# Performance work log

Hardware: AMD Instinct MI355X
Metric: run time of the kernel (lower is better)

Reference implementation:

```python
import jax, jax.numpy as jnp
import numpy as np

V_NUM = 50000
E_NUM = 10000
EMB_DIM = 128
LAYER_NUM = 2
N_INC = 600000
VE_TAU = 1.0
EV_TAU = 1.0


def _segment_softmax(a, idx, num_segments):
    # a: [N, 1], idx: [N] -> softmax within each segment (stable)
    m = jax.ops.segment_max(a, idx, num_segments=num_segments)
    ex = jnp.exp(a - m[idx])
    s = jax.ops.segment_sum(ex, idx, num_segments=num_segments)
    return ex / s[idx]


def setup_inputs() -> dict:
    key = jax.random.key(0)
    ks = jax.random.split(key, 12)
    std = (2.0 ** 0.5) * (2.0 / (EMB_DIM + 1)) ** 0.5  # xavier_normal gain sqrt(2)
    v_emb = jax.random.normal(ks[0], (V_NUM, EMB_DIM), dtype=jnp.float32)
    t_emb = jax.random.normal(ks[1], (V_NUM, EMB_DIM), dtype=jnp.float32)
    e_emb = jax.random.normal(ks[2], (E_NUM, EMB_DIM), dtype=jnp.float32)
    v_idx = jax.random.randint(ks[3], (N_INC, 1), 0, V_NUM)
    e_idx = jax.random.randint(ks[4], (N_INC, 1), 0, E_NUM)
    ve = jnp.concatenate([v_idx, e_idx], axis=1).astype(jnp.int32)
    p = lambda k: std * jax.random.normal(k, (LAYER_NUM, EMB_DIM), dtype=jnp.float32)
    return {
        "v_emb": v_emb, "t_emb": t_emb, "e_emb": e_emb, "ve": ve,
        "av_v2e": p(ks[5]), "at_v2e": p(ks[6]), "ae_v2e": p(ks[7]),
        "av_e2v": p(ks[8]), "at_e2v": p(ks[9]), "ae_e2v": p(ks[10]),
    }


def _agg(v_fea, t_fea, e_fea, v, e, av, at, ae, tau, dst_idx, dst_num, src_fea, src_idx):
    # attention logits per incidence: tanh(a_v[v] + a_t[v] + a_e[e]) / tau, shape [N, 1]
    sv = v_fea @ av[:, None]  # [V,1]
    st = t_fea @ at[:, None]  # [V,1]
    se = e_fea @ ae[:, None]  # [E,1]
    a = jnp.tanh(sv[v] + st[v] + se[e]) / tau
    a = _segment_softmax(a, dst_idx, dst_num)
    return jax.ops.segment_sum(a * src_fea[src_idx], dst_idx, num_segments=dst_num)


def reference(v_emb, t_emb, e_emb, ve, av_v2e, at_v2e, ae_v2e, av_e2v, at_e2v, ae_e2v):
    v = ve[:, 0]
    e = ve[:, 1]
    v_stack = [v_emb]
    e_stack = [e_emb]
    for l in range(LAYER_NUM):
        v_fea = v_stack[-1]
        e_fea = e_stack[-1]
        # V2E: softmax over edge segments, aggregate node features into edges
        e_new = _agg(v_fea, t_emb, e_fea, v, e, av_v2e[l], at_v2e[l], ae_v2e[l],
                     VE_TAU, e, E_NUM, v_fea, v)
        e_stack.append(jax.nn.relu(e_new))
        # E2V uses pre-relu e_new (as in original: e_fea_ not reassigned to relu)
        v_new = _agg(v_fea, t_emb, e_new, v, e, av_e2v[l], at_e2v[l], ae_e2v[l],
                     EV_TAU, v, V_NUM, e_new, e)
        v_stack.append(jax.nn.relu(v_new))
    v_out = jnp.mean(jnp.stack(v_stack, axis=1), axis=1)
    e_out = jnp.mean(jnp.stack(e_stack, axis=1), axis=1)
    return (v_out, e_out)
```

## Files before the change

### kernel.cpp

```cpp
#include <hip/hip_runtime.h>

#define DIM 128
#define VSTRIDE 48
#define ESTRIDE 128
#define NSL 128
#define DSLE 79
#define DSLV 391
#define CAPS 5440

typedef unsigned short ushort_t;
typedef unsigned int   uint_t;

__device__ inline ushort_t f2bf(float f) {
    uint_t u = __float_as_uint(f);
    u += 0x7FFF + ((u >> 16) & 1);
    return (ushort_t)(u >> 16);
}
__device__ inline float bf2f(ushort_t h) { return __uint_as_float((uint_t)h << 16); }
__device__ inline float lo16(uint_t u) { return bf2f((ushort_t)u); }
__device__ inline float hi16(uint_t u) { return bf2f((ushort_t)(u >> 16)); }

__device__ inline float wfun(float x) {
    float t = __expf(2.f * x);
    float r = __builtin_amdgcn_rcpf(t + 1.f);
    return __expf(1.f - 2.f * r);
}

__device__ inline float wred(float x) {
    #pragma unroll
    for (int o = 32; o; o >>= 1) x += __shfl_xor(x, o, 64);
    return x;
}

__global__ void k_part(const int2* __restrict__ ve, int N,
                       int* __restrict__ curE, int* __restrict__ curV,
                       uint_t* __restrict__ peE, uint_t* __restrict__ peV)
{
    __shared__ int hE[NSL], hV[NSL], baE[NSL], baV[NSL];
    int k0 = blockIdx.x * 1024;
    int k1 = min(N, k0 + 1024);
    if (threadIdx.x < NSL) { hE[threadIdx.x] = 0; }
    else if (threadIdx.x < 2 * NSL) { hV[threadIdx.x - NSL] = 0; }
    __syncthreads();
    for (int k = k0 + threadIdx.x; k < k1; k += 256) {
        int2 p = ve[k];
        atomicAdd(&hE[(uint_t)p.y / DSLE], 1);
        atomicAdd(&hV[(uint_t)p.x / DSLV], 1);
    }
    __syncthreads();
    if (threadIdx.x < NSL) {
        int t = threadIdx.x;
        baE[t] = atomicAdd(&curE[t], hE[t]); hE[t] = 0;
    } else if (threadIdx.x < 2 * NSL) {
        int t = threadIdx.x - NSL;
        baV[t] = atomicAdd(&curV[t], hV[t]); hV[t] = 0;
    }
    __syncthreads();
    for (int k = k0 + threadIdx.x; k < k1; k += 256) {
        int2 p = ve[k];
        uint_t sE = (uint_t)p.y / DSLE, sV = (uint_t)p.x / DSLV;
        int rE = baE[sE] + atomicAdd(&hE[sE], 1);
        if (rE < CAPS)
            peE[(size_t)sE * CAPS + rE] = ((uint_t)(p.y - sE * DSLE) << 16) | (uint_t)p.x;
        int rV = baV[sV] + atomicAdd(&hV[sV], 1);
        if (rV < CAPS)
            peV[(size_t)sV * CAPS + rV] = ((uint_t)(p.x - sV * DSLV) << 16) | (uint_t)p.y;
    }
}

__global__ void k_setup(const uint_t* __restrict__ peE, const uint_t* __restrict__ peV,
                        const int* __restrict__ curE, const int* __restrict__ curV,
                        int* __restrict__ cntE, int* __restrict__ cntV,
                        ushort_t* __restrict__ bE, ushort_t* __restrict__ bV,
                        const float* __restrict__ v_emb, const float* __restrict__ t_emb,
                        const float* __restrict__ e_emb,
                        const float* __restrict__ av0, const float* __restrict__ at0,
                        const float* __restrict__ av1, const float* __restrict__ at1,
                        const float* __restrict__ at2, const float* __restrict__ at3,
                        const float* __restrict__ ae0,
                        uint_t* __restrict__ vb,
                        float* __restrict__ scv0, float* __restrict__ scv1,
                        float* __restrict__ st2, float* __restrict__ st3,
                        float* __restrict__ sce0,
                        int V, int E, int gVpre)
{
    __shared__ __align__(16) ushort_t sb[DSLV * VSTRIDE];
    __shared__ int shc[DSLV];
    int b = blockIdx.x;
    if (b < 2 * NSL) {
        int isV = (b >= NSL);
        int s = isV ? b - NSL : b;
        int dsl = isV ? DSLV : DSLE;
        int stride = isV ? VSTRIDE : ESTRIDE;
        int lo = s * dsl;
        int nd = min((isV ? V : E) - lo, dsl);
        if (nd <= 0) return;
        const uint_t* pe = (isV ? peV : peE) + (size_t)s * CAPS;
        int len = (isV ? curV : curE)[s]; if (len > CAPS) len = CAPS;
        for (int t = threadIdx.x; t < nd; t += 256) shc[t] = 0;
        __syncthreads();
        for (int i = threadIdx.x; i < len; i += 256) {
            uint_t u = pe[i];
            int dl = (int)(u >> 16);
            int slot = atomicAdd(&shc[dl], 1);
            if (slot < stride) sb[dl * stride + slot] = (ushort_t)(u & 0xffffu);
        }
        __syncthreads();
        int* cnt = isV ? cntV : cntE;
        for (int t = threadIdx.x; t < nd; t += 256) cnt[lo + t] = shc[t];
        uint_t* gout = (uint_t*)((isV ? bV : bE) + (size_t)lo * stride);
        const uint_t* lsrc = (const uint_t*)sb;
        int nu = nd * stride / 2;
        for (int t = threadIdx.x; t < nu; t += 256) gout[t] = lsrc[t];
        return;
    }
    b -= 2 * NSL;
    int lane = threadIdx.x & 63;
    int wv   = threadIdx.x >> 6;
    if (b < gVpre) {
        int row = b * 4 + wv;
        if (row >= V) return;
        float2 v = ((const float2*)(v_emb + (size_t)row * DIM))[lane];
        float2 t = ((const float2*)(t_emb + (size_t)row * DIM))[lane];
        vb[(size_t)row * 64 + lane] = (uint_t)f2bf(v.x) | ((uint_t)f2bf(v.y) << 16);
        float2 a0 = ((const float2*)av0)[lane], b0 = ((const float2*)at0)[lane];
        float2 a1 = ((const float2*)av1)[lane], b1 = ((const float2*)at1)[lane];
        float2 b2 = ((const float2*)at2)[lane], b3 = ((const float2*)at3)[lane];
        float d0 = v.x * a0.x + v.y * a0.y + t.x * b0.x + t.y * b0.y;
        float d1 = v.x * a1.x + v.y * a1.y + t.x * b1.x + t.y * b1.y;
        float d2 = t.x * b2.x + t.y * b2.y;
        float d3 = t.x * b3.x + t.y * b3.y;
        d0 = wred(d0); d1 = wred(d1); d2 = wred(d2); d3 = wred(d3);
        if (lane == 0) { scv0[row] = d0; scv1[row] = d1; st2[row] = d2; st3[row] = d3; }
    } else {
        int row = (b - gVpre) * 4 + wv;
        if (row >= E) return;
        float2 v = ((const float2*)(e_emb + (size_t)row * DIM))[lane];
        float2 a = ((const float2*)ae0)[lane];
        float d = wred(v.x * a.x + v.y * a.y);
        if (lane == 0) sce0[row] = d;
    }
}

__global__ void k_gatherE(const ushort_t* __restrict__ bucket, const int* __restrict__ cnt,
                          const float* __restrict__ scSrc, const float* __restrict__ scDst,
                          const uint_t* __restrict__ src_bf,
                          float* __restrict__ outF, uint_t* __restrict__ outB, int reluB,
                          const float* __restrict__ pd0, float* __restrict__ osc0,
                          const float* __restrict__ pd1, float* __restrict__ osc1, int relu1,
                          const float* __restrict__ meanA, const float* __restrict__ meanB,
                          int ndst)
{
    __shared__ float l4[4][32][4];
    __shared__ float lw[4];
    int dst = blockIdx.x;
    if (dst >= ndst) return;
    int wv = threadIdx.x >> 6, lane = threadIdx.x & 63;
    int h = lane >> 5, c = lane & 31;
    int m = cnt[dst]; if (m > ESTRIDE) m = ESTRIDE;
    const ushort_t* s = bucket + (size_t)dst * ESTRIDE;
    float sd = scDst[dst];
    int m4 = (m + 3) >> 2;
    int j0 = wv * m4;
    int cw = min(m, j0 + m4) - j0; if (cw < 0) cw = 0;
    int   idxl = 0;
    float wl   = 0.f;
    if (lane < cw) {
        idxl = s[j0 + lane];
        wl   = wfun(scSrc[idxl] + sd);
    }
    float ws = wred(wl);
    float a0 = 0.f, a1 = 0.f, a2 = 0.f, a3 = 0.f;
    int mp = (cw + 3) & ~3;
    for (int j = 0; j < mp; j += 4) {
        int   i0 = __shfl(idxl, j + h, 64),     i1 = __shfl(idxl, j + 2 + h, 64);
        float w0 = __shfl(wl,   j + h, 64),     w1 = __shfl(wl,   j + 2 + h, 64);
        uint2 u0 = ((const uint2*)(src_bf + (size_t)i0 * 64))[c];
        uint2 u1 = ((const uint2*)(src_bf + (size_t)i1 * 64))[c];
        a0 += w0 * lo16(u0.x) + w1 * lo16(u1.x);
        a1 += w0 * hi16(u0.x) + w1 * hi16(u1.x);
        a2 += w0 * lo16(u0.y) + w1 * lo16(u1.y);
        a3 += w0 * hi16(u0.y) + w1 * hi16(u1.y);
    }
    a0 += __shfl_xor(a0, 32, 64); a1 += __shfl_xor(a1, 32, 64);
    a2 += __shfl_xor(a2, 32, 64); a3 += __shfl_xor(a3, 32, 64);
    if (lane < 32) { l4[wv][c][0] = a0; l4[wv][c][1] = a1; l4[wv][c][2] = a2; l4[wv][c][3] = a3; }
    if (lane == 0) lw[wv] = ws;
    __syncthreads();
    if (wv != 0) return;
    bool act = lane < 32;
    a0 = l4[0][c][0] + l4[1][c][0] + l4[2][c][0] + l4[3][c][0];
    a1 = l4[0][c][1] + l4[1][c][1] + l4[2][c][1] + l4[3][c][1];
    a2 = l4[0][c][2] + l4[1][c][2] + l4[2][c][2] + l4[3][c][2];
    a3 = l4[0][c][3] + l4[1][c][3] + l4[2][c][3] + l4[3][c][3];
    ws = lw[0] + lw[1] + lw[2] + lw[3];
    float inv = (ws > 0.f) ? 1.f / ws : 0.f;
    float4 r; r.x = a0 * inv; r.y = a1 * inv; r.z = a2 * inv; r.w = a3 * inv;
    if (outB && act) {
        float bx = reluB ? fmaxf(r.x, 0.f) : r.x, by = reluB ? fmaxf(r.y, 0.f) : r.y;
        float bz = reluB ? fmaxf(r.z, 0.f) : r.z, bw = reluB ? fmaxf(r.w, 0.f) : r.w;
        uint2 u; u.x = (uint_t)f2bf(bx) | ((uint_t)f2bf(by) << 16);
        u.y = (uint_t)f2bf(bz) | ((uint_t)f2bf(bw) << 16);
        ((uint2*)(outB + (size_t)dst * 64))[c] = u;
    }
    if (pd0) {
        float4 q = ((const float4*)pd0)[c];
        float d = act ? (r.x * q.x + r.y * q.y + r.z * q.z + r.w * q.w) : 0.f;
        d = wred(d);
        if (lane == 0) osc0[dst] = d;
    }
    if (pd1) {
        float x0 = relu1 ? fmaxf(r.x, 0.f) : r.x, x1 = relu1 ? fmaxf(r.y, 0.f) : r.y;
        float x2 = relu1 ? fmaxf(r.z, 0.f) : r.z, x3 = relu1 ? fmaxf(r.w, 0.f) : r.w;
        float4 q = ((const float4*)pd1)[c];
        float d = act ? (x0 * q.x + x1 * q.y + x2 * q.z + x3 * q.w) : 0.f;
        d = wred(d);
        if (lane == 0) osc1[dst] = d;
    }
    if (meanA) {
        float4 ma = ((const float4*)(meanA + (size_t)dst * DIM))[c];
        float4 mb = ((const float4*)(meanB + (size_t)dst * DIM))[c];
        r.x = (ma.x + fmaxf(mb.x, 0.f) + fmaxf(r.x, 0.f)) * (1.f / 3.f);
        r.y = (ma.y + fmaxf(mb.y, 0.f) + fmaxf(r.y, 0.f)) * (1.f / 3.f);
        r.z = (ma.z + fmaxf(mb.z, 0.f) + fmaxf(r.z, 0.f)) * (1.f / 3.f);
        r.w = (ma.w + fmaxf(mb.w, 0.f) + fmaxf(r.w, 0.f)) * (1.f / 3.f);
    }
    if (act) ((float4*)(outF + (size_t)dst * DIM))[c] = r;
}

__global__ void k_gatherV(const ushort_t* __restrict__ bucket, const int* __restrict__ cnt,
                          const float* __restrict__ scSrc, const float* __restrict__ scDst,
                          const uint_t* __restrict__ src_bf,
                          float* __restrict__ outF, uint_t* __restrict__ outB, int reluB,
                          const float* __restrict__ pd0, const float* __restrict__ sta0,
                          float* __restrict__ osc0, int relu0,
                          const float* __restrict__ pd1, const float* __restrict__ sta1,
                          float* __restrict__ osc1, int relu1,
                          const float* __restrict__ meanA, const float* __restrict__ meanB,
                          int ndst)
{
    int dst  = blockIdx.x * 4 + (threadIdx.x >> 6);
    int lane = threadIdx.x & 63;
    int h = lane >> 5, c = lane & 31;
    if (dst >= ndst) return;
    int m = cnt[dst]; if (m > VSTRIDE) m = VSTRIDE;
    const ushort_t* s = bucket + (size_t)dst * VSTRIDE;
    float sd = scDst[dst];
    int   idxl = 0;
    float wl   = 0.f;
    if (lane < m) {
        idxl = s[lane];
        wl   = wfun(scSrc[idxl] + sd);
    }
    float ws = wred(wl);
    float a0 = 0.f, a1 = 0.f, a2 = 0.f, a3 = 0.f;
    int mp = (m + 3) & ~3;
    for (int j = 0; j < mp; j += 4) {
        int   i0 = __shfl(idxl, j + h, 64),     i1 = __shfl(idxl, j + 2 + h, 64);
        float w0 = __shfl(wl,   j + h, 64),     w1 = __shfl(wl,   j + 2 + h, 64);
        uint2 u0 = ((const uint2*)(src_bf + (size_t)i0 * 64))[c];
        uint2 u1 = ((const uint2*)(src_bf + (size_t)i1 * 64))[c];
        a0 += w0 * lo16(u0.x) + w1 * lo16(u1.x);
        a1 += w0 * hi16(u0.x) + w1 * hi16(u1.x);
        a2 += w0 * lo16(u0.y) + w1 * lo16(u1.y);
        a3 += w0 * hi16(u0.y) + w1 * hi16(u1.y);
    }
    a0 += __shfl_xor(a0, 32, 64); a1 += __shfl_xor(a1, 32, 64);
    a2 += __shfl_xor(a2, 32, 64); a3 += __shfl_xor(a3, 32, 64);
    bool act = lane < 32;
    float inv = (ws > 0.f) ? 1.f / ws : 0.f;
    float4 r; r.x = a0 * inv; r.y = a1 * inv; r.z = a2 * inv; r.w = a3 * inv;
    if (outB && act) {
        float bx = reluB ? fmaxf(r.x, 0.f) : r.x, by = reluB ? fmaxf(r.y, 0.f) : r.y;
        float bz = reluB ? fmaxf(r.z, 0.f) : r.z, bw = reluB ? fmaxf(r.w, 0.f) : r.w;
        uint2 u; u.x = (uint_t)f2bf(bx) | ((uint_t)f2bf(by) << 16);
        u.y = (uint_t)f2bf(bz) | ((uint_t)f2bf(bw) << 16);
        ((uint2*)(outB + (size_t)dst * 64))[c] = u;
    }
    if (pd0) {
        float x0 = relu0 ? fmaxf(r.x, 0.f) : r.x, x1 = relu0 ? fmaxf(r.y, 0.f) : r.y;
        float x2 = relu0 ? fmaxf(r.z, 0.f) : r.z, x3 = relu0 ? fmaxf(r.w, 0.f) : r.w;
        float4 q = ((const float4*)pd0)[c];
        float d = act ? (x0 * q.x + x1 * q.y + x2 * q.z + x3 * q.w) : 0.f;
        d = wred(d);
        if (lane == 0) osc0[dst] = d + (sta0 ? sta0[dst] : 0.f);
    }
    if (pd1) {
        float x0 = relu1 ? fmaxf(r.x, 0.f) : r.x, x1 = relu1 ? fmaxf(r.y, 0.f) : r.y;
        float x2 = relu1 ? fmaxf(r.z, 0.f) : r.z, x3 = relu1 ? fmaxf(r.w, 0.f) : r.w;
        float4 q = ((const float4*)pd1)[c];
        float d = act ? (x0 * q.x + x1 * q.y + x2 * q.z + x3 * q.w) : 0.f;
        d = wred(d);
        if (lane == 0) osc1[dst] = d + (sta1 ? sta1[dst] : 0.f);
    }
    if (meanA) {
        float4 ma = ((const float4*)(meanA + (size_t)dst * DIM))[c];
        float4 mb = ((const float4*)(meanB + (size_t)dst * DIM))[c];
        r.x = (ma.x + fmaxf(mb.x, 0.f) + fmaxf(r.x, 0.f)) * (1.f / 3.f);
        r.y = (ma.y + fmaxf(mb.y, 0.f) + fmaxf(r.y, 0.f)) * (1.f / 3.f);
        r.z = (ma.z + fmaxf(mb.z, 0.f) + fmaxf(r.z, 0.f)) * (1.f / 3.f);
        r.w = (ma.w + fmaxf(mb.w, 0.f) + fmaxf(r.w, 0.f)) * (1.f / 3.f);
    }
    if (act) ((float4*)(outF + (size_t)dst * DIM))[c] = r;
}

extern "C" void kernel_launch(void* const* d_in, const int* in_sizes, int n_in,
                              void* d_out, int out_size, void* d_ws, size_t ws_size,
                              hipStream_t stream)
{
    const float* v_emb  = (const float*)d_in[0];
    const float* t_emb  = (const float*)d_in[1];
    const float* e_emb  = (const float*)d_in[2];
    const int2*  ve     = (const int2*)d_in[3];
    const float* av_v2e = (const float*)d_in[4];
    const float* at_v2e = (const float*)d_in[5];
    const float* ae_v2e = (const float*)d_in[6];
    const float* av_e2v = (const float*)d_in[7];
    const float* at_e2v = (const float*)d_in[8];
    const float* ae_e2v = (const float*)d_in[9];

    const int V = in_sizes[0] / DIM;
    const int E = in_sizes[2] / DIM;
    const int N = in_sizes[3] / 2;

    char* p = (char*)d_ws;
    auto alloc = [&](size_t bytes) { char* r = p; p += (bytes + 255) & ~(size_t)255; return r; };
    float* v_new0 = (float*)alloc((size_t)V * DIM * 4);
    float* e_new0 = (float*)alloc((size_t)E * DIM * 4);
    uint_t* vb    = (uint_t*)alloc((size_t)V * 64 * 4);
    uint_t* eb    = (uint_t*)alloc((size_t)E * 64 * 4);
    ushort_t* bV  = (ushort_t*)alloc((size_t)V * VSTRIDE * 2);
    ushort_t* bE  = (ushort_t*)alloc((size_t)E * ESTRIDE * 2);
    uint_t* peE   = (uint_t*)alloc((size_t)NSL * CAPS * 4);
    uint_t* peV   = (uint_t*)alloc((size_t)NSL * CAPS * 4);
    int*   cntV   = (int*)alloc((size_t)(V + E + 2 * NSL) * 4);
    int*   cntE   = cntV + V;
    int*   curE   = cntE + E;
    int*   curV   = curE + NSL;
    float* scv0   = (float*)alloc((size_t)V * 4);
    float* scv1   = (float*)alloc((size_t)V * 4);
    float* scv2   = (float*)alloc((size_t)V * 4);
    float* scv3   = (float*)alloc((size_t)V * 4);
    float* st2    = (float*)alloc((size_t)V * 4);
    float* st3    = (float*)alloc((size_t)V * 4);
    float* sce0   = (float*)alloc((size_t)E * 4);
    float* sce1   = (float*)alloc((size_t)E * 4);
    float* sce2   = (float*)alloc((size_t)E * 4);
    float* sce3   = (float*)alloc((size_t)E * 4);

    float* out_v = (float*)d_out;
    float* out_e = out_v + (size_t)V * DIM;

    hipMemsetAsync(curE, 0, (size_t)2 * NSL * 4, stream);

    k_part<<<(N + 1023) / 1024, 256, 0, stream>>>(ve, N, curE, curV, peE, peV);

    const int gVpre = (V + 3) / 4, gEpre = (E + 3) / 4;
    k_setup<<<2 * NSL + gVpre + gEpre, 256, 0, stream>>>(
        peE, peV, curE, curV, cntE, cntV, bE, bV,
        v_emb, t_emb, e_emb,
        av_v2e, at_v2e, av_e2v, at_e2v, at_v2e + DIM, at_e2v + DIM, ae_v2e,
        vb, scv0, scv1, st2, st3, sce0, V, E, gVpre);

    k_gatherE<<<E, 256, 0, stream>>>(bE, cntE, scv0, sce0, vb,
        e_new0, eb, 0, ae_e2v, sce1, ae_v2e + DIM, sce2, 1,
        nullptr, nullptr, E);

    k_gatherV<<<(V + 3) / 4, 256, 0, stream>>>(bV, cntV, sce1, scv1, eb,
        v_new0, vb, 1,
        av_v2e + DIM, st2, scv2, 1,
        av_e2v + DIM, st3, scv3, 1,
        nullptr, nullptr, V);

    k_gatherE<<<E, 256, 0, stream>>>(bE, cntE, scv2, sce2, vb,
        out_e, eb, 0, ae_e2v + DIM, sce3, nullptr, nullptr, 0,
        e_emb, e_new0, E);

    k_gatherV<<<(V + 3) / 4, 256, 0, stream>>>(bV, cntV, sce3, scv3, eb,
        out_v, nullptr, 0,
        nullptr, nullptr, nullptr, 0,
        nullptr, nullptr, nullptr, 0,
        v_emb, v_new0, V);
}
```

Before: 171.7 us.

## Remap gather kernels: one wave per edge, two vertices per wave

The edge gather now gives each edge a single wavefront instead of a 256-thread block. Each lane holds up to two incidences, which removes the shared-memory cross-wave reduction and the block barrier. The vertex gather now processes two vertices per wavefront with interleaved loads, raising memory-level parallelism and amortising per-wave setup. The shared epilogue moves into a helper function. Risks: the edge path is now serialized over about 60 incidences per wave, and two accumulator sets raise register pressure.

```diff
diff --git a/kernel.cpp b/kernel.cpp
--- a/kernel.cpp
+++ b/kernel.cpp
@@ -142,6 +142,49 @@
     }
 }
 
+__device__ inline void epilog(int dst, int lane, int c, float4 r,
+                              float* __restrict__ outF, uint_t* __restrict__ outB, int reluB,
+                              const float* __restrict__ pd0, const float* __restrict__ sta0,
+                              float* __restrict__ osc0, int relu0,
+                              const float* __restrict__ pd1, const float* __restrict__ sta1,
+                              float* __restrict__ osc1, int relu1,
+                              const float* __restrict__ meanA, const float* __restrict__ meanB)
+{
+    bool act = lane < 32;
+    if (outB && act) {
+        float bx = reluB ? fmaxf(r.x, 0.f) : r.x, by = reluB ? fmaxf(r.y, 0.f) : r.y;
+        float bz = reluB ? fmaxf(r.z, 0.f) : r.z, bw = reluB ? fmaxf(r.w, 0.f) : r.w;
+        uint2 u; u.x = (uint_t)f2bf(bx) | ((uint_t)f2bf(by) << 16);
+        u.y = (uint_t)f2bf(bz) | ((uint_t)f2bf(bw) << 16);
+        ((uint2*)(outB + (size_t)dst * 64))[c] = u;
+    }
+    if (pd0) {
+        float x0 = relu0 ? fmaxf(r.x, 0.f) : r.x, x1 = relu0 ? fmaxf(r.y, 0.f) : r.y;
+        float x2 = relu0 ? fmaxf(r.z, 0.f) : r.z, x3 = relu0 ? fmaxf(r.w, 0.f) : r.w;
+        float4 q = ((const float4*)pd0)[c];
+        float d = act ? (x0 * q.x + x1 * q.y + x2 * q.z + x3 * q.w) : 0.f;
+        d = wred(d);
+        if (lane == 0) osc0[dst] = d + (sta0 ? sta0[dst] : 0.f);
+    }
+    if (pd1) {
+        float x0 = relu1 ? fmaxf(r.x, 0.f) : r.x, x1 = relu1 ? fmaxf(r.y, 0.f) : r.y;
+        float x2 = relu1 ? fmaxf(r.z, 0.f) : r.z, x3 = relu1 ? fmaxf(r.w, 0.f) : r.w;
+        float4 q = ((const float4*)pd1)[c];
+        float d = act ? (x0 * q.x + x1 * q.y + x2 * q.z + x3 * q.w) : 0.f;
+        d = wred(d);
+        if (lane == 0) osc1[dst] = d + (sta1 ? sta1[dst] : 0.f);
+    }
+    if (meanA) {
+        float4 ma = ((const float4*)(meanA + (size_t)dst * DIM))[c];
+        float4 mb = ((const float4*)(meanB + (size_t)dst * DIM))[c];
+        r.x = (ma.x + fmaxf(mb.x, 0.f) + fmaxf(r.x, 0.f)) * (1.f / 3.f);
+        r.y = (ma.y + fmaxf(mb.y, 0.f) + fmaxf(r.y, 0.f)) * (1.f / 3.f);
+        r.z = (ma.z + fmaxf(mb.z, 0.f) + fmaxf(r.z, 0.f)) * (1.f / 3.f);
+        r.w = (ma.w + fmaxf(mb.w, 0.f) + fmaxf(r.w, 0.f)) * (1.f / 3.f);
+    }
+    if (act) ((float4*)(outF + (size_t)dst * DIM))[c] = r;
+}
+
 __global__ void k_gatherE(const ushort_t* __restrict__ bucket, const int* __restrict__ cnt,
                           const float* __restrict__ scSrc, const float* __restrict__ scDst,
                           const uint_t* __restrict__ src_bf,
@@ -151,81 +194,43 @@
                           const float* __restrict__ meanA, const float* __restrict__ meanB,
                           int ndst)
 {
-    __shared__ float l4[4][32][4];
-    __shared__ float lw[4];
-    int dst = blockIdx.x;
+    int dst  = blockIdx.x * 4 + (threadIdx.x >> 6);
+    int lane = threadIdx.x & 63;
+    int h = lane >> 5, c = lane & 31;
     if (dst >= ndst) return;
-    int wv = threadIdx.x >> 6, lane = threadIdx.x & 63;
-    int h = lane >> 5, c = lane & 31;
     int m = cnt[dst]; if (m > ESTRIDE) m = ESTRIDE;
     const ushort_t* s = bucket + (size_t)dst * ESTRIDE;
     float sd = scDst[dst];
-    int m4 = (m + 3) >> 2;
-    int j0 = wv * m4;
-    int cw = min(m, j0 + m4) - j0; if (cw < 0) cw = 0;
-    int   idxl = 0;
-    float wl   = 0.f;
-    if (lane < cw) {
-        idxl = s[j0 + lane];
-        wl   = wfun(scSrc[idxl] + sd);
-    }
-    float ws = wred(wl);
+    int idx0 = 0, idx1 = 0;
+    float w0l = 0.f, w1l = 0.f;
+    if (lane < m)      { idx0 = s[lane];      w0l = wfun(scSrc[idx0] + sd); }
+    if (64 + lane < m) { idx1 = s[64 + lane]; w1l = wfun(scSrc[idx1] + sd); }
+    float ws = wred(w0l + w1l);
     float a0 = 0.f, a1 = 0.f, a2 = 0.f, a3 = 0.f;
-    int mp = (cw + 3) & ~3;
+    int mp = (m + 3) & ~3;
     for (int j = 0; j < mp; j += 4) {
-        int   i0 = __shfl(idxl, j + h, 64),     i1 = __shfl(idxl, j + 2 + h, 64);
-        float w0 = __shfl(wl,   j + h, 64),     w1 = __shfl(wl,   j + 2 + h, 64);
-        uint2 u0 = ((const uint2*)(src_bf + (size_t)i0 * 64))[c];
-        uint2 u1 = ((const uint2*)(src_bf + (size_t)i1 * 64))[c];
-        a0 += w0 * lo16(u0.x) + w1 * lo16(u1.x);
-        a1 += w0 * hi16(u0.x) + w1 * hi16(u1.x);
-        a2 += w0 * lo16(u0.y) + w1 * lo16(u1.y);
-        a3 += w0 * hi16(u0.y) + w1 * hi16(u1.y);
+        int jj = j & 63;
+        int ia, ib; float wa, wb;
+        if (j < 64) {
+            ia = __shfl(idx0, jj + h, 64);     wa = __shfl(w0l, jj + h, 64);
+            ib = __shfl(idx0, jj + 2 + h, 64); wb = __shfl(w0l, jj + 2 + h, 64);
+        } else {
+            ia = __shfl(idx1, jj + h, 64);     wa = __shfl(w1l, jj + h, 64);
+            ib = __shfl(idx1, jj + 2 + h, 64); wb = __shfl(w1l, jj + 2 + h, 64);
+        }
+        uint2 u0 = ((const uint2*)(src_bf + (size_t)ia * 64))[c];
+        uint2 u1 = ((const uint2*)(src_bf + (size_t)ib * 64))[c];
+        a0 += wa * lo16(u0.x) + wb * lo16(u1.x);
+        a1 += wa * hi16(u0.x) + wb * hi16(u1.x);
+        a2 += wa * lo16(u0.y) + wb * lo16(u1.y);
+        a3 += wa * hi16(u0.y) + wb * hi16(u1.y);
     }
     a0 += __shfl_xor(a0, 32, 64); a1 += __shfl_xor(a1, 32, 64);
     a2 += __shfl_xor(a2, 32, 64); a3 += __shfl_xor(a3, 32, 64);
-    if (lane < 32) { l4[wv][c][0] = a0; l4[wv][c][1] = a1; l4[wv][c][2] = a2; l4[wv][c][3] = a3; }
-    if (lane == 0) lw[wv] = ws;
-    __syncthreads();
-    if (wv != 0) return;
-    bool act = lane < 32;
-    a0 = l4[0][c][0] + l4[1][c][0] + l4[2][c][0] + l4[3][c][0];
-    a1 = l4[0][c][1] + l4[1][c][1] + l4[2][c][1] + l4[3][c][1];
-    a2 = l4[0][c][2] + l4[1][c][2] + l4[2][c][2] + l4[3][c][2];
-    a3 = l4[0][c][3] + l4[1][c][3] + l4[2][c][3] + l4[3][c][3];
-    ws = lw[0] + lw[1] + lw[2] + lw[3];
     float inv = (ws > 0.f) ? 1.f / ws : 0.f;
     float4 r; r.x = a0 * inv; r.y = a1 * inv; r.z = a2 * inv; r.w = a3 * inv;
-    if (outB && act) {
-        float bx = reluB ? fmaxf(r.x, 0.f) : r.x, by = reluB ? fmaxf(r.y, 0.f) : r.y;
-        float bz = reluB ? fmaxf(r.z, 0.f) : r.z, bw = reluB ? fmaxf(r.w, 0.f) : r.w;
-        uint2 u; u.x = (uint_t)f2bf(bx) | ((uint_t)f2bf(by) << 16);
-        u.y = (uint_t)f2bf(bz) | ((uint_t)f2bf(bw) << 16);
-        ((uint2*)(outB + (size_t)dst * 64))[c] = u;
-    }
-    if (pd0) {
-        float4 q = ((const float4*)pd0)[c];
-        float d = act ? (r.x * q.x + r.y * q.y + r.z * q.z + r.w * q.w) : 0.f;
-        d = wred(d);
-        if (lane == 0) osc0[dst] = d;
-    }
-    if (pd1) {
-        float x0 = relu1 ? fmaxf(r.x, 0.f) : r.x, x1 = relu1 ? fmaxf(r.y, 0.f) : r.y;
-        float x2 = relu1 ? fmaxf(r.z, 0.f) : r.z, x3 = relu1 ? fmaxf(r.w, 0.f) : r.w;
-        float4 q = ((const float4*)pd1)[c];
-        float d = act ? (x0 * q.x + x1 * q.y + x2 * q.z + x3 * q.w) : 0.f;
-        d = wred(d);
-        if (lane == 0) osc1[dst] = d;
-    }
-    if (meanA) {
-        float4 ma = ((const float4*)(meanA + (size_t)dst * DIM))[c];
-        float4 mb = ((const float4*)(meanB + (size_t)dst * DIM))[c];
-        r.x = (ma.x + fmaxf(mb.x, 0.f) + fmaxf(r.x, 0.f)) * (1.f / 3.f);
-        r.y = (ma.y + fmaxf(mb.y, 0.f) + fmaxf(r.y, 0.f)) * (1.f / 3.f);
-        r.z = (ma.z + fmaxf(mb.z, 0.f) + fmaxf(r.z, 0.f)) * (1.f / 3.f);
-        r.w = (ma.w + fmaxf(mb.w, 0.f) + fmaxf(r.w, 0.f)) * (1.f / 3.f);
-    }
-    if (act) ((float4*)(outF + (size_t)dst * DIM))[c] = r;
+    epilog(dst, lane, c, r, outF, outB, reluB,
+           pd0, nullptr, osc0, 0, pd1, nullptr, osc1, relu1, meanA, meanB);
 }
 
 __global__ void k_gatherV(const ushort_t* __restrict__ bucket, const int* __restrict__ cnt,
@@ -239,69 +244,59 @@
                           const float* __restrict__ meanA, const float* __restrict__ meanB,
                           int ndst)
 {
-    int dst  = blockIdx.x * 4 + (threadIdx.x >> 6);
+    int wv   = threadIdx.x >> 6;
     int lane = threadIdx.x & 63;
     int h = lane >> 5, c = lane & 31;
-    if (dst >= ndst) return;
-    int m = cnt[dst]; if (m > VSTRIDE) m = VSTRIDE;
-    const ushort_t* s = bucket + (size_t)dst * VSTRIDE;
-    float sd = scDst[dst];
-    int   idxl = 0;
-    float wl   = 0.f;
-    if (lane < m) {
-        idxl = s[lane];
-        wl   = wfun(scSrc[idxl] + sd);
-    }
-    float ws = wred(wl);
-    float a0 = 0.f, a1 = 0.f, a2 = 0.f, a3 = 0.f;
-    int mp = (m + 3) & ~3;
+    int dA = blockIdx.x * 8 + wv * 2;
+    int dB = dA + 1;
+    if (dA >= ndst) return;
+    bool hasB = dB < ndst;
+    int mA = cnt[dA]; if (mA > VSTRIDE) mA = VSTRIDE;
+    int mB = hasB ? cnt[dB] : 0; if (mB > VSTRIDE) mB = VSTRIDE;
+    const ushort_t* sA = bucket + (size_t)dA * VSTRIDE;
+    const ushort_t* sB = bucket + (size_t)dB * VSTRIDE;
+    float sdA = scDst[dA];
+    float sdB = hasB ? scDst[dB] : 0.f;
+    int idxA = 0, idxB = 0;
+    float wA = 0.f, wB = 0.f;
+    if (lane < mA) { idxA = sA[lane]; wA = wfun(scSrc[idxA] + sdA); }
+    if (lane < mB) { idxB = sB[lane]; wB = wfun(scSrc[idxB] + sdB); }
+    float wsA = wred(wA), wsB = wred(wB);
+    float aA0 = 0.f, aA1 = 0.f, aA2 = 0.f, aA3 = 0.f;
+    float aB0 = 0.f, aB1 = 0.f, aB2 = 0.f, aB3 = 0.f;
+    int mp = max((mA + 3) & ~3, (mB + 3) & ~3);
     for (int j = 0; j < mp; j += 4) {
-        int   i0 = __shfl(idxl, j + h, 64),     i1 = __shfl(idxl, j + 2 + h, 64);
-        float w0 = __shfl(wl,   j + h, 64),     w1 = __shfl(wl,   j + 2 + h, 64);
-        uint2 u0 = ((const uint2*)(src_bf + (size_t)i0 * 64))[c];
-        uint2 u1 = ((const uint2*)(src_bf + (size_t)i1 * 64))[c];
-        a0 += w0 * lo16(u0.x) + w1 * lo16(u1.x);
-        a1 += w0 * hi16(u0.x) + w1 * hi16(u1.x);
-        a2 += w0 * lo16(u0.y) + w1 * lo16(u1.y);
-        a3 += w0 * hi16(u0.y) + w1 * hi16(u1.y);
-    }
-    a0 += __shfl_xor(a0, 32, 64); a1 += __shfl_xor(a1, 32, 64);
-    a2 += __shfl_xor(a2, 32, 64); a3 += __shfl_xor(a3, 32, 64);
-    bool act = lane < 32;
-    float inv = (ws > 0.f) ? 1.f / ws : 0.f;
-    float4 r; r.x = a0 * inv; r.y = a1 * inv; r.z = a2 * inv; r.w = a3 * inv;
-    if (outB && act) {
-        float bx = reluB ? fmaxf(r.x, 0.f) : r.x, by = reluB ? fmaxf(r.y, 0.f) : r.y;
-        float bz = reluB ? fmaxf(r.z, 0.f) : r.z, bw = reluB ? fmaxf(r.w, 0.f) : r.w;
-        uint2 u; u.x = (uint_t)f2bf(bx) | ((uint_t)f2bf(by) << 16);
-        u.y = (uint_t)f2bf(bz) | ((uint_t)f2bf(bw) << 16);
-        ((uint2*)(outB + (size_t)dst * 64))[c] = u;
-    }
-    if (pd0) {
-        float x0 = relu0 ? fmaxf(r.x, 0.f) : r.x, x1 = relu0 ? fmaxf(r.y, 0.f) : r.y;
-        float x2 = relu0 ? fmaxf(r.z, 0.f) : r.z, x3 = relu0 ? fmaxf(r.w, 0.f) : r.w;
-        float4 q = ((const float4*)pd0)[c];
-        float d = act ? (x0 * q.x + x1 * q.y + x2 * q.z + x3 * q.w) : 0.f;
-        d = wred(d);
-        if (lane == 0) osc0[dst] = d + (sta0 ? sta0[dst] : 0.f);
-    }
-    if (pd1) {
-        float x0 = relu1 ? fmaxf(r.x, 0.f) : r.x, x1 = relu1 ? fmaxf(r.y, 0.f) : r.y;
-        float x2 = relu1 ? fmaxf(r.z, 0.f) : r.z, x3 = relu1 ? fmaxf(r.w, 0.f) : r.w;
-        float4 q = ((const float4*)pd1)[c];
-        float d = act ? (x0 * q.x + x1 * q.y + x2 * q.z + x3 * q.w) : 0.f;
-        d = wred(d);
-        if (lane == 0) osc1[dst] = d + (sta1 ? sta1[dst] : 0.f);
-    }
-    if (meanA) {
-        float4 ma = ((const float4*)(meanA + (size_t)dst * DIM))[c];
-        float4 mb = ((const float4*)(meanB + (size_t)dst * DIM))[c];
-        r.x = (ma.x + fmaxf(mb.x, 0.f) + fmaxf(r.x, 0.f)) * (1.f / 3.f);
-        r.y = (ma.y + fmaxf(mb.y, 0.f) + fmaxf(r.y, 0.f)) * (1.f / 3.f);
-        r.z = (ma.z + fmaxf(mb.z, 0.f) + fmaxf(r.z, 0.f)) * (1.f / 3.f);
-        r.w = (ma.w + fmaxf(mb.w, 0.f) + fmaxf(r.w, 0.f)) * (1.f / 3.f);
-    }
-    if (act) ((float4*)(outF + (size_t)dst * DIM))[c] = r;
+        int   iA0 = __shfl(idxA, j + h, 64),     iA1 = __shfl(idxA, j + 2 + h, 64);
+        float vA0 = __shfl(wA,   j + h, 64),     vA1 = __shfl(wA,   j + 2 + h, 64);
+        int   iB0 = __shfl(idxB, j + h, 64),     iB1 = __shfl(idxB, j + 2 + h, 64);
+        float vB0 = __shfl(wB,   j + h, 64),     vB1 = __shfl(wB,   j + 2 + h, 64);
+        uint2 uA0 = ((const uint2*)(src_bf + (size_t)iA0 * 64))[c];
+        uint2 uA1 = ((const uint2*)(src_bf + (size_t)iA1 * 64))[c];
+        uint2 uB0 = ((const uint2*)(src_bf + (size_t)iB0 * 64))[c];
+        uint2 uB1 = ((const uint2*)(src_bf + (size_t)iB1 * 64))[c];
+        aA0 += vA0 * lo16(uA0.x) + vA1 * lo16(uA1.x);
+        aA1 += vA0 * hi16(uA0.x) + vA1 * hi16(uA1.x);
+        aA2 += vA0 * lo16(uA0.y) + vA1 * lo16(uA1.y);
+        aA3 += vA0 * hi16(uA0.y) + vA1 * hi16(uA1.y);
+        aB0 += vB0 * lo16(uB0.x) + vB1 * lo16(uB1.x);
+        aB1 += vB0 * hi16(uB0.x) + vB1 * hi16(uB1.x);
+        aB2 += vB0 * lo16(uB0.y) + vB1 * lo16(uB1.y);
+        aB3 += vB0 * hi16(uB0.y) + vB1 * hi16(uB1.y);
+    }
+    aA0 += __shfl_xor(aA0, 32, 64); aA1 += __shfl_xor(aA1, 32, 64);
+    aA2 += __shfl_xor(aA2, 32, 64); aA3 += __shfl_xor(aA3, 32, 64);
+    aB0 += __shfl_xor(aB0, 32, 64); aB1 += __shfl_xor(aB1, 32, 64);
+    aB2 += __shfl_xor(aB2, 32, 64); aB3 += __shfl_xor(aB3, 32, 64);
+    float invA = (wsA > 0.f) ? 1.f / wsA : 0.f;
+    float4 rA; rA.x = aA0 * invA; rA.y = aA1 * invA; rA.z = aA2 * invA; rA.w = aA3 * invA;
+    epilog(dA, lane, c, rA, outF, outB, reluB,
+           pd0, sta0, osc0, relu0, pd1, sta1, osc1, relu1, meanA, meanB);
+    if (hasB) {
+        float invB = (wsB > 0.f) ? 1.f / wsB : 0.f;
+        float4 rB; rB.x = aB0 * invB; rB.y = aB1 * invB; rB.z = aB2 * invB; rB.w = aB3 * invB;
+        epilog(dB, lane, c, rB, outF, outB, reluB,
+               pd0, sta0, osc0, relu0, pd1, sta1, osc1, relu1, meanA, meanB);
+    }
 }
 
 extern "C" void kernel_launch(void* const* d_in, const int* in_sizes, int n_in,
@@ -362,21 +357,21 @@
         av_v2e, at_v2e, av_e2v, at_e2v, at_v2e + DIM, at_e2v + DIM, ae_v2e,
         vb, scv0, scv1, st2, st3, sce0, V, E, gVpre);
 
-    k_gatherE<<<E, 256, 0, stream>>>(bE, cntE, scv0, sce0, vb,
+    k_gatherE<<<(E + 3) / 4, 256, 0, stream>>>(bE, cntE, scv0, sce0, vb,
         e_new0, eb, 0, ae_e2v, sce1, ae_v2e + DIM, sce2, 1,
         nullptr, nullptr, E);
 
-    k_gatherV<<<(V + 3) / 4, 256, 0, stream>>>(bV, cntV, sce1, scv1, eb,
+    k_gatherV<<<(V + 7) / 8, 256, 0, stream>>>(bV, cntV, sce1, scv1, eb,
         v_new0, vb, 1,
         av_v2e + DIM, st2, scv2, 1,
         av_e2v + DIM, st3, scv3, 1,
         nullptr, nullptr, V);
 
-    k_gatherE<<<E, 256, 0, stream>>>(bE, cntE, scv2, sce2, vb,
+    k_gatherE<<<(E + 3) / 4, 256, 0, stream>>>(bE, cntE, scv2, sce2, vb,
         out_e, eb, 0, ae_e2v + DIM, sce3, nullptr, nullptr, 0,
         e_emb, e_new0, E);
 
-    k_gatherV<<<(V + 3) / 4, 256, 0, stream>>>(bV, cntV, sce3, scv3, eb,
+    k_gatherV<<<(V + 7) / 8, 256, 0, stream>>>(bV, cntV, sce3, scv3, eb,
         out_v, nullptr, 0,
         nullptr, nullptr, nullptr, 0,
         nullptr, nullptr, nullptr, 0,
```

After: 172.8 us. About the same (+0.6%).
